# Optimization experiments

Hardware: AMD Instinct MI355X
Metric: run time of the kernel (lower is better)

## Reference

```python
import jax, jax.numpy as jnp
import numpy as np

MODEL_DIM = 1024
NUM_HEADS = 16
DEPTH = MODEL_DIM // NUM_HEADS


def setup_inputs() -> dict:
    key = jax.random.key(0)
    ks = jax.random.split(key, 9)
    B, S, D = 4, 2048, MODEL_DIM
    scale = 1.0 / np.sqrt(D)
    x = jax.random.normal(ks[0], (B, S, D), dtype=jnp.float32)
    wq = jax.random.normal(ks[1], (D, D), dtype=jnp.float32) * scale
    bq = jnp.zeros((D,), dtype=jnp.float32)
    wk = jax.random.normal(ks[2], (D, D), dtype=jnp.float32) * scale
    bk = jnp.zeros((D,), dtype=jnp.float32)
    wv = jax.random.normal(ks[3], (D, D), dtype=jnp.float32) * scale
    bv = jnp.zeros((D,), dtype=jnp.float32)
    wo = jax.random.normal(ks[4], (D, D), dtype=jnp.float32) * scale
    bo = jnp.zeros((D,), dtype=jnp.float32)
    return {"x": x, "wq": wq, "bq": bq, "wk": wk, "bk": bk,
            "wv": wv, "bv": bv, "wo": wo, "bo": bo}


def reference(x, wq, bq, wk, bk, wv, bv, wo, bo):
    B, S, D = x.shape
    H, dh = NUM_HEADS, DEPTH
    # projections
    q = (x @ wq + bq).reshape(B, S, H, dh).transpose(0, 2, 1, 3)  # [B,H,S,dh]
    k = (x @ wk + bk).reshape(B, S, H, dh).transpose(0, 2, 1, 3)
    v = (x @ wv + bv).reshape(B, S, H, dh).transpose(0, 2, 1, 3)
    # scaled dot-product attention (full score matrix, as in source)
    logits = jnp.einsum('bhqd,bhkd->bhqk', q, k) / jnp.sqrt(jnp.float32(dh))
    attn = jax.nn.softmax(logits, axis=-1)
    out = jnp.einsum('bhqk,bhkd->bhqd', attn, v)  # [B,H,S,dh]
    out = out.transpose(0, 2, 1, 3).reshape(B, S, D)
    return out @ wo + bo
```

## Files before the change

kernel.cpp:

```cpp
#include <hip/hip_runtime.h>
#include <hip/hip_bf16.h>


#define S_LEN 2048
#define DMODEL 1024
#define NH 16
#define DH 64
#define BATCH 4
#define MROWS (BATCH * S_LEN)
#define NELEM_X (MROWS * DMODEL)
#define NELEM_W (DMODEL * DMODEL)
#define NELEM_B DMODEL

typedef short short8 __attribute__((ext_vector_type(8)));
typedef float floatx4 __attribute__((ext_vector_type(4)));

__device__ __forceinline__ float bf2f(unsigned short u) {
    union { unsigned int i; float f; } c; c.i = ((unsigned int)u) << 16; return c.f;
}
__device__ __forceinline__ unsigned int f2bf_pk(float lo, float hi) {
    unsigned int r;
    asm("v_cvt_pk_bf16_f32 %0, %1, %2" : "=v"(r) : "v"(lo), "v"(hi));
    return r;
}
__device__ __forceinline__ void async_copy16(const void* g, void* l) {
    __builtin_amdgcn_global_load_lds(
        (const __attribute__((address_space(1))) unsigned int*)g,
        (__attribute__((address_space(3))) unsigned int*)l, 16, 0, 0);
}

__global__ void sniff_kernel(const unsigned short* __restrict__ x, int* flag) {
    __shared__ int cnt;
    if (threadIdx.x == 0) cnt = 0;
    __syncthreads();
    int c = 0;
    for (int i = threadIdx.x; i < 65536; i += 256) {
        unsigned int e = (x[i] >> 7) & 0xFFu;
        if (e >= 0xC0u) c++;
    }
    atomicAdd(&cnt, c);
    __syncthreads();
    if (threadIdx.x == 0) *flag = (cnt > 64) ? 1 : 0;
}

struct ConvArgs { const void* s[5]; unsigned short* d[5]; int n8[5]; };
__global__ void convert_all(ConvArgs a, const int* __restrict__ flag) {
    const int seg = blockIdx.y;
    const int f = *flag;
    const int n8 = a.n8[seg];
    unsigned short* dst = a.d[seg];
    int i = blockIdx.x * blockDim.x + threadIdx.x;
    const int stride = gridDim.x * blockDim.x;
    if (f) {
        const float4* s4 = (const float4*)a.s[seg];
        for (; i < n8; i += stride) {
            float4 x0 = s4[2 * i], x1 = s4[2 * i + 1];
            uint4 o;
            o.x = f2bf_pk(x0.x, x0.y); o.y = f2bf_pk(x0.z, x0.w);
            o.z = f2bf_pk(x1.x, x1.y); o.w = f2bf_pk(x1.z, x1.w);
            *(uint4*)(dst + (size_t)i * 8) = o;
        }
    } else {
        const uint4* s4 = (const uint4*)a.s[seg];
        for (; i < n8; i += stride) *(uint4*)(dst + (size_t)i * 8) = s4[i];
    }
}

struct TWArgs { const void* s[4]; unsigned short* d[4]; };
__global__ void transpose_w(TWArgs a, const int* __restrict__ flag) {
    __shared__ unsigned int Lt[64 * 33];
    const int z = blockIdx.z;
    const int f = *flag;
    const int k0 = blockIdx.x * 64, n0 = blockIdx.y * 64;
    const int t = threadIdx.x;
    const int c = t & 63, rgrp = t >> 6;

    if (f) {
        const float* W = (const float*)a.s[z];
        #pragma unroll
        for (int s = 0; s < 8; s++) {
            int r0 = rgrp * 16 + 2 * s;
            float v0 = W[(size_t)(k0 + r0) * DMODEL + n0 + c];
            float v1 = W[(size_t)(k0 + r0 + 1) * DMODEL + n0 + c];
            Lt[c * 33 + rgrp * 8 + s] = f2bf_pk(v0, v1);
        }
    } else {
        const unsigned short* W = (const unsigned short*)a.s[z];
        #pragma unroll
        for (int s = 0; s < 8; s++) {
            int r0 = rgrp * 16 + 2 * s;
            unsigned int lo = W[(size_t)(k0 + r0) * DMODEL + n0 + c];
            unsigned int hi = W[(size_t)(k0 + r0 + 1) * DMODEL + n0 + c];
            Lt[c * 33 + rgrp * 8 + s] = lo | (hi << 16);
        }
    }
    __syncthreads();
    const int row = t >> 2, j = t & 3;
    unsigned int* outp = (unsigned int*)(a.d[z] + (size_t)(n0 + row) * DMODEL + k0);
    #pragma unroll
    for (int i = 0; i < 8; i++) outp[j * 8 + i] = Lt[row * 33 + j * 8 + i];
}

__global__ void transpose_v(const unsigned short* __restrict__ vws,
                            unsigned short* __restrict__ vt) {
    __shared__ unsigned int Lt[64 * 33];
    const int tok0 = blockIdx.x * 64;
    const int bh   = blockIdx.y;
    const int b    = bh >> 4;
    const int h    = bh & 15;
    const int t = threadIdx.x;
    const int c = t & 63, rgrp = t >> 6;

    const unsigned short* src = vws + (size_t)b * S_LEN * DMODEL + h * DH;
    #pragma unroll
    for (int s = 0; s < 8; s++) {
        int r0 = rgrp * 16 + 2 * s;
        unsigned int lo = src[(size_t)(tok0 + r0) * DMODEL + c];
        unsigned int hi = src[(size_t)(tok0 + r0 + 1) * DMODEL + c];
        Lt[c * 33 + rgrp * 8 + s] = lo | (hi << 16);
    }
    __syncthreads();
    const int row = t >> 2, j = t & 3;
    unsigned int* outp = (unsigned int*)(vt + (size_t)bh * DH * S_LEN
                                            + (size_t)row * S_LEN + tok0);
    #pragma unroll
    for (int i = 0; i < 8; i++) outp[j * 8 + i] = Lt[row * 33 + j * 8 + i];
}

__global__ __launch_bounds__(256, 2)
void gemm_bias_kernel(const unsigned short* __restrict__ X,
                      const unsigned short* __restrict__ T0, const unsigned short* __restrict__ B0, void* __restrict__ Y0,
                      const unsigned short* __restrict__ T1, const unsigned short* __restrict__ B1, void* __restrict__ Y1,
                      const unsigned short* __restrict__ T2, const unsigned short* __restrict__ B2, void* __restrict__ Y2,
                      float os0, float os1, float os2,
                      const int* __restrict__ flag, int fp32_out)
{
    const unsigned short* Wt = T0; const unsigned short* Bi = B0; void* Y = Y0;
    float os = os0;
    if (blockIdx.z == 1) { Wt = T1; Bi = B1; Y = Y1; os = os1; }
    else if (blockIdx.z == 2) { Wt = T2; Bi = B2; Y = Y2; os = os2; }
    const int f32o = fp32_out ? (*flag) : 0;

    __shared__ __align__(16) unsigned short As[128 * 32];
    __shared__ __align__(16) unsigned short Bs[128 * 32];

    const int t    = threadIdx.x;
    const int lane = t & 63;
    const int wid  = t >> 6;
    const int quad = lane >> 4;
    const int n16  = lane & 15;
    const int wm   = wid >> 1, wn = wid & 1;

    const int m0 = blockIdx.x * 128;
    const int n0 = blockIdx.y * 128;

    floatx4 acc[4][4];
    #pragma unroll
    for (int i = 0; i < 4; i++)
        #pragma unroll
        for (int j = 0; j < 4; j++) acc[i][j] = (floatx4){0.f, 0.f, 0.f, 0.f};

    const int r = t >> 2, c8 = (t & 3) * 8;

    for (int kb = 0; kb < DMODEL; kb += 32) {
        __syncthreads();
        async_copy16(X  + (size_t)(m0 + r)      * DMODEL + kb + c8, As + r * 32 + c8);
        async_copy16(X  + (size_t)(m0 + 64 + r) * DMODEL + kb + c8, As + (64 + r) * 32 + c8);
        async_copy16(Wt + (size_t)(n0 + r)      * DMODEL + kb + c8, Bs + r * 32 + c8);
        async_copy16(Wt + (size_t)(n0 + 64 + r) * DMODEL + kb + c8, Bs + (64 + r) * 32 + c8);
        __syncthreads();

        short8 af[4], bfr[4];
        #pragma unroll
        for (int mt = 0; mt < 4; mt++)
            af[mt] = *(const short8*)(As + (wm * 64 + mt * 16 + n16) * 32 + quad * 8);
        #pragma unroll
        for (int nt = 0; nt < 4; nt++)
            bfr[nt] = *(const short8*)(Bs + (wn * 64 + nt * 16 + n16) * 32 + quad * 8);
        #pragma unroll
        for (int mt = 0; mt < 4; mt++)
            #pragma unroll
            for (int nt = 0; nt < 4; nt++)
                acc[mt][nt] = __builtin_amdgcn_mfma_f32_16x16x32_bf16(af[mt], bfr[nt], acc[mt][nt], 0, 0, 0);
    }

    float bv4[4];
    #pragma unroll
    for (int nt = 0; nt < 4; nt++) bv4[nt] = bf2f(Bi[n0 + wn * 64 + nt * 16 + n16]) * os;
    #pragma unroll
    for (int mt = 0; mt < 4; mt++)
        #pragma unroll
        for (int rr = 0; rr < 4; rr++) {
            size_t row = (size_t)(m0 + wm * 64 + mt * 16 + quad * 4 + rr);
            if (f32o) {
                #pragma unroll
                for (int nt = 0; nt < 4; nt++) {
                    int col = n0 + wn * 64 + nt * 16 + n16;
                    ((float*)Y)[row * DMODEL + col] = fmaf(acc[mt][nt][rr], os, bv4[nt]);
                }
            } else {
                #pragma unroll
                for (int np = 0; np < 2; np++) {
                    float v0 = fmaf(acc[mt][2 * np    ][rr], os, bv4[2 * np]);
                    float v1 = fmaf(acc[mt][2 * np + 1][rr], os, bv4[2 * np + 1]);
                    unsigned int pk = f2bf_pk(v0, v1);
                    int col = n0 + wn * 64 + (2 * np) * 16 + n16;
                    ((unsigned short*)Y)[row * DMODEL + col]      = (unsigned short)pk;
                    ((unsigned short*)Y)[row * DMODEL + col + 16] = (unsigned short)(pk >> 16);
                }
            }
        }
}

__global__ __launch_bounds__(256, 2)
void attn_kernel(const unsigned short* Qw,
                 const unsigned short* __restrict__ Kw,
                 const unsigned short* __restrict__ VT,
                 unsigned short* Ow)
{
    __shared__ __align__(16) unsigned short Ks[64 * 72];
    __shared__ __align__(16) unsigned short Vts[64 * 72];
    __shared__ __align__(16) unsigned short Ps[4 * 16 * 72];

    const int t    = threadIdx.x;
    const int lane = t & 63;
    const int w    = t >> 6;
    const int quad = lane >> 4;
    const int n16  = lane & 15;

    const int bid  = blockIdx.x;
    const int bh   = bid & 63;
    const int qblk = bid >> 6;
    const int b    = bh >> 4;
    const int h    = bh & 15;

    const size_t baseRow = (size_t)b * S_LEN;
    const int hoff = h * DH;
    const unsigned short* VTb = VT + (size_t)bh * DH * S_LEN;

    int qrow[4];
    short8 qf[4][2];
    #pragma unroll
    for (int g = 0; g < 4; g++) {
        qrow[g] = qblk * 256 + w * 64 + g * 16 + n16;
        qf[g][0] = *(const short8*)(Qw + (baseRow + qrow[g]) * DMODEL + hoff + quad * 8);
        qf[g][1] = *(const short8*)(Qw + (baseRow + qrow[g]) * DMODEL + hoff + 32 + quad * 8);
    }

    floatx4 acco[4][4];
    #pragma unroll
    for (int g = 0; g < 4; g++)
        #pragma unroll
        for (int i = 0; i < 4; i++) acco[g][i] = (floatx4){0.f, 0.f, 0.f, 0.f};
    float ls[4] = {0.f, 0.f, 0.f, 0.f};

    const int krow = t >> 3, kchk = (t & 7) * 8;
    const int vrow = t >> 2, vchk = (t & 3) * 16;

    for (int kb = 0; kb < S_LEN; kb += 64) {
        __syncthreads();
        *(float4*)(Ks + krow * 72 + kchk) =
            *(const float4*)(Kw + (baseRow + kb + krow) * DMODEL + hoff + kchk);
        *(float4*)(Ks + (krow + 32) * 72 + kchk) =
            *(const float4*)(Kw + (baseRow + kb + krow + 32) * DMODEL + hoff + kchk);
        *(float4*)(Vts + vrow * 72 + vchk) =
            *(const float4*)(VTb + (size_t)vrow * S_LEN + kb + vchk);
        *(float4*)(Vts + vrow * 72 + vchk + 8) =
            *(const float4*)(VTb + (size_t)vrow * S_LEN + kb + vchk + 8);
        __syncthreads();

        floatx4 sf[4][4];
        #pragma unroll
        for (int g = 0; g < 4; g++)
            #pragma unroll
            for (int kt = 0; kt < 4; kt++) sf[g][kt] = (floatx4){0.f, 0.f, 0.f, 0.f};
        #pragma unroll
        for (int kt = 0; kt < 4; kt++)
            #pragma unroll
            for (int ks = 0; ks < 2; ks++) {
                short8 kf = *(const short8*)(Ks + (kt * 16 + n16) * 72 + ks * 32 + quad * 8);
                #pragma unroll
                for (int g = 0; g < 4; g++)
                    sf[g][kt] = __builtin_amdgcn_mfma_f32_16x16x32_bf16(kf, qf[g][ks], sf[g][kt], 0, 0, 0);
            }

        unsigned short* Pw = Ps + w * 16 * 72;
        unsigned int*   Pu = (unsigned int*)Pw;
        short8 pf[4][2];
        #pragma unroll
        for (int g = 0; g < 4; g++) {
            float lsum = 0.f;
            #pragma unroll
            for (int kt = 0; kt < 4; kt++)
                #pragma unroll
                for (int rr = 0; rr < 4; rr++) {
                    float p = __builtin_exp2f(sf[g][kt][rr]);
                    sf[g][kt][rr] = p;
                    lsum += p;
                }
            ls[g] += lsum;
            #pragma unroll
            for (int kt = 0; kt < 4; kt++) {
                uint2 pk2 = make_uint2(f2bf_pk(sf[g][kt][0], sf[g][kt][1]),
                                       f2bf_pk(sf[g][kt][2], sf[g][kt][3]));
                *(uint2*)(Pu + n16 * 36 + kt * 8 + quad * 2) = pk2;
            }
            __asm__ volatile("" ::: "memory");
            pf[g][0] = *(const short8*)(Pw + n16 * 72 + quad * 8);
            pf[g][1] = *(const short8*)(Pw + n16 * 72 + 32 + quad * 8);
            __asm__ volatile("" ::: "memory");
        }

        #pragma unroll
        for (int ks = 0; ks < 2; ks++)
            #pragma unroll
            for (int dt = 0; dt < 4; dt++) {
                short8 vf = *(const short8*)(Vts + (dt * 16 + n16) * 72 + ks * 32 + quad * 8);
                #pragma unroll
                for (int g = 0; g < 4; g++)
                    acco[g][dt] = __builtin_amdgcn_mfma_f32_16x16x32_bf16(vf, pf[g][ks], acco[g][dt], 0, 0, 0);
            }
    }

    #pragma unroll
    for (int g = 0; g < 4; g++) {
        float l = ls[g];
        l += __shfl_xor(l, 16);
        l += __shfl_xor(l, 32);
        const float rinv = 1.f / l;
        #pragma unroll
        for (int dt = 0; dt < 4; dt++) {
            uint2 o;
            o.x = f2bf_pk(acco[g][dt][0] * rinv, acco[g][dt][1] * rinv);
            o.y = f2bf_pk(acco[g][dt][2] * rinv, acco[g][dt][3] * rinv);
            *(uint2*)(Ow + (baseRow + qrow[g]) * DMODEL + hoff + dt * 16 + quad * 4) = o;
        }
    }
}

extern "C" void kernel_launch(void* const* d_in, const int* in_sizes, int n_in,
                              void* d_out, int out_size, void* d_ws, size_t ws_size,
                              hipStream_t stream)
{
    unsigned short* base = (unsigned short*)d_ws;
    int* flag = (int*)d_ws;
    unsigned short* xc  = base + 8;
    unsigned short* wqt = xc  + NELEM_X;
    unsigned short* wkt = wqt + NELEM_W;
    unsigned short* wvt = wkt + NELEM_W;
    unsigned short* wot = wvt + NELEM_W;
    unsigned short* bqc = wot + NELEM_W;
    unsigned short* bkc = bqc + NELEM_B;
    unsigned short* bvc = bkc + NELEM_B;
    unsigned short* boc = bvc + NELEM_B;
    unsigned short* qws = boc + NELEM_B;
    unsigned short* kws = qws + NELEM_X;
    unsigned short* vws = kws + NELEM_X;
    unsigned short* aws = qws;
    unsigned short* vtw = xc;

    sniff_kernel<<<1, 256, 0, stream>>>((const unsigned short*)d_in[0], flag);

    ConvArgs ca;
    const void* csrc[5] = {d_in[0], d_in[2], d_in[4], d_in[6], d_in[8]};
    unsigned short* cdst[5] = {xc, bqc, bkc, bvc, boc};
    int cn8[5] = {NELEM_X / 8, NELEM_B / 8, NELEM_B / 8, NELEM_B / 8, NELEM_B / 8};
    for (int i = 0; i < 5; i++) { ca.s[i] = csrc[i]; ca.d[i] = cdst[i]; ca.n8[i] = cn8[i]; }
    convert_all<<<dim3(256, 5), 256, 0, stream>>>(ca, flag);

    TWArgs tw;
    const void* tsrc[4] = {d_in[1], d_in[3], d_in[5], d_in[7]};
    unsigned short* tdst[4] = {wqt, wkt, wvt, wot};
    for (int i = 0; i < 4; i++) { tw.s[i] = tsrc[i]; tw.d[i] = tdst[i]; }
    transpose_w<<<dim3(16, 16, 4), 256, 0, stream>>>(tw, flag);

    const float qscale = 0.125f * 1.44269504088896340736f;
    gemm_bias_kernel<<<dim3(64, 8, 3), 256, 0, stream>>>(
        xc, wqt, bqc, qws, wkt, bkc, kws, wvt, bvc, vws,
        qscale, 1.f, 1.f, flag, 0);

    transpose_v<<<dim3(32, 64), 256, 0, stream>>>(vws, vtw);

    attn_kernel<<<dim3(512), 256, 0, stream>>>(qws, kws, vtw, aws);

    gemm_bias_kernel<<<dim3(64, 8, 1), 256, 0, stream>>>(
        aws, wot, boc, d_out, wot, boc, d_out, wot, boc, d_out,
        1.f, 1.f, 1.f, flag, 1);
}
```

Measured before the change: 388.7 us.

## Fold softmax row sums into PV MFMA and remap GEMM blocks per XCD

The attention kernel adds an extra V tile of rows filled with bf16 ones (plus zeros), so the PV MFMA also produces the row sum of P. This removes the per-element scalar summation and the cross-lane shuffles in exchange for one more MFMA column tile per k-step and more registers. P staging now uses a separate LDS buffer per query group, so all exp/pack writes can finish before the reads, dropping the interleaved barriers but using more LDS. The GEMM launch is flattened to a 1D grid where the low bits of the block id select the N tile, so blocks sharing a weight tile land on the same XCD for L2 reuse.

```diff
diff --git a/kernel.cpp b/kernel.cpp
--- a/kernel.cpp
+++ b/kernel.cpp
@@ -133,12 +133,19 @@
                       const unsigned short* __restrict__ T1, const unsigned short* __restrict__ B1, void* __restrict__ Y1,
                       const unsigned short* __restrict__ T2, const unsigned short* __restrict__ B2, void* __restrict__ Y2,
                       float os0, float os1, float os2,
-                      const int* __restrict__ flag, int fp32_out)
+                      const int* __restrict__ flag, int fp32_out, int zmul)
 {
+    const int bid = blockIdx.x;
+    const int xcd = bid & 7;
+    const int idx = bid >> 3;
+    const int z   = idx % zmul;
+    const int m0  = (idx / zmul) * 128;
+    const int n0  = xcd * 128;
+
     const unsigned short* Wt = T0; const unsigned short* Bi = B0; void* Y = Y0;
     float os = os0;
-    if (blockIdx.z == 1) { Wt = T1; Bi = B1; Y = Y1; os = os1; }
-    else if (blockIdx.z == 2) { Wt = T2; Bi = B2; Y = Y2; os = os2; }
+    if (z == 1) { Wt = T1; Bi = B1; Y = Y1; os = os1; }
+    else if (z == 2) { Wt = T2; Bi = B2; Y = Y2; os = os2; }
     const int f32o = fp32_out ? (*flag) : 0;
 
     __shared__ __align__(16) unsigned short As[128 * 32];
@@ -150,9 +157,6 @@
     const int quad = lane >> 4;
     const int n16  = lane & 15;
     const int wm   = wid >> 1, wn = wid & 1;
-
-    const int m0 = blockIdx.x * 128;
-    const int n0 = blockIdx.y * 128;
 
     floatx4 acc[4][4];
     #pragma unroll
@@ -219,8 +223,8 @@
                  unsigned short* Ow)
 {
     __shared__ __align__(16) unsigned short Ks[64 * 72];
-    __shared__ __align__(16) unsigned short Vts[64 * 72];
-    __shared__ __align__(16) unsigned short Ps[4 * 16 * 72];
+    __shared__ __align__(16) unsigned short Vts[80 * 72];
+    __shared__ __align__(16) unsigned short Ps[4 * 4 * 16 * 72];
 
     const int t    = threadIdx.x;
     const int lane = t & 63;
@@ -238,6 +242,12 @@
     const int hoff = h * DH;
     const unsigned short* VTb = VT + (size_t)bh * DH * S_LEN;
 
+    {
+        unsigned int* Vu = (unsigned int*)Vts;
+        for (int i = 2304 + t; i < 2880; i += 256)
+            Vu[i] = (i < 2340) ? 0x3F803F80u : 0u;
+    }
+
     int qrow[4];
     short8 qf[4][2];
     #pragma unroll
@@ -247,12 +257,11 @@
         qf[g][1] = *(const short8*)(Qw + (baseRow + qrow[g]) * DMODEL + hoff + 32 + quad * 8);
     }
 
-    floatx4 acco[4][4];
+    floatx4 acco[4][5];
     #pragma unroll
     for (int g = 0; g < 4; g++)
         #pragma unroll
-        for (int i = 0; i < 4; i++) acco[g][i] = (floatx4){0.f, 0.f, 0.f, 0.f};
-    float ls[4] = {0.f, 0.f, 0.f, 0.f};
+        for (int i = 0; i < 5; i++) acco[g][i] = (floatx4){0.f, 0.f, 0.f, 0.f};
 
     const int krow = t >> 3, kchk = (t & 7) * 8;
     const int vrow = t >> 2, vchk = (t & 3) * 16;
@@ -284,37 +293,33 @@
                     sf[g][kt] = __builtin_amdgcn_mfma_f32_16x16x32_bf16(kf, qf[g][ks], sf[g][kt], 0, 0, 0);
             }
 
-        unsigned short* Pw = Ps + w * 16 * 72;
-        unsigned int*   Pu = (unsigned int*)Pw;
-        short8 pf[4][2];
         #pragma unroll
         for (int g = 0; g < 4; g++) {
-            float lsum = 0.f;
-            #pragma unroll
-            for (int kt = 0; kt < 4; kt++)
-                #pragma unroll
-                for (int rr = 0; rr < 4; rr++) {
-                    float p = __builtin_exp2f(sf[g][kt][rr]);
-                    sf[g][kt][rr] = p;
-                    lsum += p;
-                }
-            ls[g] += lsum;
+            unsigned int* Pu = (unsigned int*)(Ps + (w * 4 + g) * 16 * 72);
             #pragma unroll
             for (int kt = 0; kt < 4; kt++) {
-                uint2 pk2 = make_uint2(f2bf_pk(sf[g][kt][0], sf[g][kt][1]),
-                                       f2bf_pk(sf[g][kt][2], sf[g][kt][3]));
+                float p0 = __builtin_exp2f(sf[g][kt][0]);
+                float p1 = __builtin_exp2f(sf[g][kt][1]);
+                float p2 = __builtin_exp2f(sf[g][kt][2]);
+                float p3 = __builtin_exp2f(sf[g][kt][3]);
+                uint2 pk2 = make_uint2(f2bf_pk(p0, p1), f2bf_pk(p2, p3));
                 *(uint2*)(Pu + n16 * 36 + kt * 8 + quad * 2) = pk2;
             }
-            __asm__ volatile("" ::: "memory");
+        }
+        __asm__ volatile("" ::: "memory");
+
+        short8 pf[4][2];
+        #pragma unroll
+        for (int g = 0; g < 4; g++) {
+            const unsigned short* Pw = Ps + (w * 4 + g) * 16 * 72;
             pf[g][0] = *(const short8*)(Pw + n16 * 72 + quad * 8);
             pf[g][1] = *(const short8*)(Pw + n16 * 72 + 32 + quad * 8);
-            __asm__ volatile("" ::: "memory");
         }
 
         #pragma unroll
         for (int ks = 0; ks < 2; ks++)
             #pragma unroll
-            for (int dt = 0; dt < 4; dt++) {
+            for (int dt = 0; dt < 5; dt++) {
                 short8 vf = *(const short8*)(Vts + (dt * 16 + n16) * 72 + ks * 32 + quad * 8);
                 #pragma unroll
                 for (int g = 0; g < 4; g++)
@@ -324,9 +329,7 @@
 
     #pragma unroll
     for (int g = 0; g < 4; g++) {
-        float l = ls[g];
-        l += __shfl_xor(l, 16);
-        l += __shfl_xor(l, 32);
+        float l = __shfl(acco[g][4][0], n16);
         const float rinv = 1.f / l;
         #pragma unroll
         for (int dt = 0; dt < 4; dt++) {
@@ -375,15 +378,15 @@
     transpose_w<<<dim3(16, 16, 4), 256, 0, stream>>>(tw, flag);
 
     const float qscale = 0.125f * 1.44269504088896340736f;
-    gemm_bias_kernel<<<dim3(64, 8, 3), 256, 0, stream>>>(
+    gemm_bias_kernel<<<1536, 256, 0, stream>>>(
         xc, wqt, bqc, qws, wkt, bkc, kws, wvt, bvc, vws,
-        qscale, 1.f, 1.f, flag, 0);
+        qscale, 1.f, 1.f, flag, 0, 3);
 
     transpose_v<<<dim3(32, 64), 256, 0, stream>>>(vws, vtw);
 
     attn_kernel<<<dim3(512), 256, 0, stream>>>(qws, kws, vtw, aws);
 
-    gemm_bias_kernel<<<dim3(64, 8, 1), 256, 0, stream>>>(
+    gemm_bias_kernel<<<512, 256, 0, stream>>>(
         aws, wot, boc, d_out, wot, boc, d_out, wot, boc, d_out,
-        1.f, 1.f, 1.f, flag, 1);
-}
+        1.f, 1.f, 1.f, flag, 1, 1);
+}
```

New measurement: 389.8 us. About the same (+0.3%).
